# Performance work log

Hardware: AMD Instinct MI355X
Metric: run time of the kernel (lower is better)

Reference implementation:

```python
import jax, jax.numpy as jnp
import numpy as np


def _build_levels():
    # build_power_value(B=4): w_bit=5 -> B=4 additive-powers-of-two codebook
    value_a = [0.0] + [2.0 ** (-2 * i - 1) for i in range(3)]
    value_b = [0.0] + [2.0 ** (-2 * i - 2) for i in range(3)]
    sums = sorted({a + b for a in value_a for b in value_b})
    levels = np.asarray(sums, dtype=np.float32)
    return jnp.asarray(levels / levels.max())  # 16 levels in [0, 1]


def setup_inputs() -> dict:
    key = jax.random.key(0)
    weight = jax.random.normal(key, (4096, 4096), dtype=jnp.float32) * 0.05
    wgt_alpha = jnp.asarray(2.0, dtype=jnp.float32)
    return {"weight": weight, "wgt_alpha": wgt_alpha}


def reference(weight, wgt_alpha):
    levels = _build_levels()
    # stats are computed on weight.data in torch (detached)
    mean = jax.lax.stop_gradient(jnp.mean(weight))
    std = jax.lax.stop_gradient(jnp.std(weight, ddof=1))  # torch .std() is unbiased
    wn = (weight - mean) / std
    x = wn / wgt_alpha
    xc = jnp.clip(x, -1.0, 1.0)
    sign = jnp.sign(xc)
    # nearest-level search over the 16-entry codebook (first-min tie-break like torch)
    idx = jnp.argmin(jnp.abs(jnp.abs(xc)[..., None] - levels), axis=-1)
    q = levels[idx] * sign
    return q * wgt_alpha
```

## Files before the change

### kernel.cpp

```cpp
#include <hip/hip_runtime.h>
#include <math.h>

#define THREADS 256

typedef float f2v __attribute__((ext_vector_type(2)));
typedef float f4v __attribute__((ext_vector_type(4)));

static constexpr float kLvl[16] = {
    0.0f      / 0.75f, 0.015625f / 0.75f, 0.03125f / 0.75f, 0.046875f / 0.75f,
    0.0625f   / 0.75f, 0.09375f  / 0.75f, 0.125f   / 0.75f, 0.140625f / 0.75f,
    0.1875f   / 0.75f, 0.25f     / 0.75f, 0.28125f / 0.75f, 0.375f    / 0.75f,
    0.5f      / 0.75f, 0.515625f / 0.75f, 0.5625f  / 0.75f, 0.75f     / 0.75f,
};
static constexpr double kMid[15] = {
    ((double)kLvl[0]  + (double)kLvl[1])  * 0.5, ((double)kLvl[1]  + (double)kLvl[2])  * 0.5,
    ((double)kLvl[2]  + (double)kLvl[3])  * 0.5, ((double)kLvl[3]  + (double)kLvl[4])  * 0.5,
    ((double)kLvl[4]  + (double)kLvl[5])  * 0.5, ((double)kLvl[5]  + (double)kLvl[6])  * 0.5,
    ((double)kLvl[6]  + (double)kLvl[7])  * 0.5, ((double)kLvl[7]  + (double)kLvl[8])  * 0.5,
    ((double)kLvl[8]  + (double)kLvl[9])  * 0.5, ((double)kLvl[9]  + (double)kLvl[10]) * 0.5,
    ((double)kLvl[10] + (double)kLvl[11]) * 0.5, ((double)kLvl[11] + (double)kLvl[12]) * 0.5,
    ((double)kLvl[12] + (double)kLvl[13]) * 0.5, ((double)kLvl[13] + (double)kLvl[14]) * 0.5,
    ((double)kLvl[14] + (double)kLvl[15]) * 0.5,
};

__device__ __forceinline__ float tree64(float v) {
    #pragma unroll
    for (int m = 1; m <= 32; m <<= 1)
        v += __shfl_xor(v, m, 64);
    return v;
}

__device__ __forceinline__ float sgpr_bcast(float x) {
    return __uint_as_float(__builtin_amdgcn_readfirstlane(__float_as_uint(x)));
}

template<int PASS>
__global__ __launch_bounds__(THREADS) void leaf_pass(const float* __restrict__ w,
                                                     const float* __restrict__ bprev,
                                                     float* __restrict__ bout,
                                                     long long n, int nb) {
    #pragma clang fp contract(off)
    __shared__ float ws4[4];
    __shared__ float smean;
    float mean = 0.0f;
    if (PASS == 1) {
        int i0 = threadIdx.x * 8;
        float v = 0.0f;
        if (i0 + 7 < nb) {
            const float* p = bprev + i0;
            v = ((p[0] + p[1]) + (p[2] + p[3])) + ((p[4] + p[5]) + (p[6] + p[7]));
        }
        v = tree64(v);
        if ((threadIdx.x & 63) == 0) ws4[threadIdx.x >> 6] = v;
        __syncthreads();
        if (threadIdx.x == 0)
            smean = ((ws4[0] + ws4[1]) + (ws4[2] + ws4[3])) / (float)n;
        __syncthreads();
        mean = smean;
    }

    const long long base = (long long)blockIdx.x * 8192
                         + (long long)(threadIdx.x >> 2) * 128
                         + (long long)(threadIdx.x & 3) * 2;
    const f2v* p = (const f2v*)(w + base);
    float s0, s1;
    {
        f2v a = p[0];
        if (PASS == 1) { float x = a.x - mean, y = a.y - mean; s0 = x * x; s1 = y * y; }
        else           { s0 = a.x; s1 = a.y; }
    }
    #pragma unroll
    for (int t = 1; t < 16; ++t) {
        f2v a = p[4 * t];
        if (PASS == 1) { float x = a.x - mean, y = a.y - mean; s0 += x * x; s1 += y * y; }
        else           { s0 += a.x; s1 += a.y; }
    }
    float s = s0 + s1;
    s = tree64(s);
    if ((threadIdx.x & 63) == 0) ws4[threadIdx.x >> 6] = s;
    __syncthreads();
    if (threadIdx.x == 0)
        bout[blockIdx.x] = (ws4[0] + ws4[1]) + (ws4[2] + ws4[3]);
}

#define QSEL(V, RES) do {                                   \
    float _u  = (V) - mean;                                 \
    float _au = fabsf(_u);                                  \
    float _o  = c0;                                         \
    _o = (_au < t0)  ? _o : c1;                             \
    _o = (_au < t1)  ? _o : c2;                             \
    _o = (_au < t2)  ? _o : c3;                             \
    _o = (_au < t3)  ? _o : c4;                             \
    _o = (_au < t4)  ? _o : c5;                             \
    _o = (_au < t5)  ? _o : c6;                             \
    _o = (_au < t6)  ? _o : c7;                             \
    _o = (_au < t7)  ? _o : c8;                             \
    _o = (_au < t8)  ? _o : c9;                             \
    _o = (_au < t9)  ? _o : c10;                            \
    _o = (_au < t10) ? _o : c11;                            \
    _o = (_au < t11) ? _o : c12;                            \
    _o = (_au < t12) ? _o : c13;                            \
    _o = (_au < t13) ? _o : c14;                            \
    _o = (_au < t14) ? _o : c15;                            \
    RES = copysignf(_o, _u);                                \
} while (0)

__global__ __launch_bounds__(THREADS) void quantize_k(const f4v* __restrict__ w4,
                                                      f4v* __restrict__ o4,
                                                      const float* __restrict__ bout0,
                                                      const float* __restrict__ bout1,
                                                      const float* __restrict__ alpha_ptr,
                                                      long long n, int nb) {
    #pragma clang fp contract(off)
    __shared__ float wsA[4], wsB[4];
    __shared__ float sP[2];
    __shared__ float sT[15];
    __shared__ float sC[16];
    {
        int i0 = threadIdx.x * 8;
        float v = 0.0f, u = 0.0f;
        if (i0 + 7 < nb) {
            const float* p0 = bout0 + i0;
            const float* p1 = bout1 + i0;
            v = ((p0[0] + p0[1]) + (p0[2] + p0[3])) + ((p0[4] + p0[5]) + (p0[6] + p0[7]));
            u = ((p1[0] + p1[1]) + (p1[2] + p1[3])) + ((p1[4] + p1[5]) + (p1[6] + p1[7]));
        }
        v = tree64(v);
        u = tree64(u);
        if ((threadIdx.x & 63) == 0) { wsA[threadIdx.x >> 6] = v; wsB[threadIdx.x >> 6] = u; }
        __syncthreads();
        if (threadIdx.x == 0) {
            sP[0] = ((wsA[0] + wsA[1]) + (wsA[2] + wsA[3])) / (float)n;
            sP[1] = sqrtf(((wsB[0] + wsB[1]) + (wsB[2] + wsB[3])) / (float)(n - 1));
        }
        __syncthreads();
    }
    const float sd = sP[1];
    const float al = alpha_ptr[0];
    if (threadIdx.x < 15) {
        const double mid = kMid[threadIdx.x];
        unsigned lo = 0u, hi = 0x7F800000u;
        while (lo < hi) {
            unsigned m = (lo + hi) >> 1;
            float uu = __uint_as_float(m);
            float y  = uu / sd;
            float x  = y / al;
            float xc = fminf(x, 1.0f);
            if ((double)xc > mid) hi = m; else lo = m + 1;
        }
        sT[threadIdx.x] = __uint_as_float(lo);
    } else if (threadIdx.x < 31) {
        int i = threadIdx.x - 15;
        sC[i] = kLvl[i] * al;
    } else if (threadIdx.x == 31) {
        sC[0] = 0.0f;
    }
    __syncthreads();

    const float mean = sgpr_bcast(sP[0]);
    const float t0  = sgpr_bcast(sT[0]),  t1  = sgpr_bcast(sT[1]);
    const float t2  = sgpr_bcast(sT[2]),  t3  = sgpr_bcast(sT[3]);
    const float t4  = sgpr_bcast(sT[4]),  t5  = sgpr_bcast(sT[5]);
    const float t6  = sgpr_bcast(sT[6]),  t7  = sgpr_bcast(sT[7]);
    const float t8  = sgpr_bcast(sT[8]),  t9  = sgpr_bcast(sT[9]);
    const float t10 = sgpr_bcast(sT[10]), t11 = sgpr_bcast(sT[11]);
    const float t12 = sgpr_bcast(sT[12]), t13 = sgpr_bcast(sT[13]);
    const float t14 = sgpr_bcast(sT[14]);
    const float c0  = sgpr_bcast(sC[0]),  c1  = sgpr_bcast(sC[1]);
    const float c2  = sgpr_bcast(sC[2]),  c3  = sgpr_bcast(sC[3]);
    const float c4  = sgpr_bcast(sC[4]),  c5  = sgpr_bcast(sC[5]);
    const float c6  = sgpr_bcast(sC[6]),  c7  = sgpr_bcast(sC[7]);
    const float c8  = sgpr_bcast(sC[8]),  c9  = sgpr_bcast(sC[9]);
    const float c10 = sgpr_bcast(sC[10]), c11 = sgpr_bcast(sC[11]);
    const float c12 = sgpr_bcast(sC[12]), c13 = sgpr_bcast(sC[13]);
    const float c14 = sgpr_bcast(sC[14]), c15 = sgpr_bcast(sC[15]);

    long long n4     = n >> 2;
    long long tid    = (long long)blockIdx.x * THREADS + threadIdx.x;
    long long stride = (long long)gridDim.x * THREADS;

    long long i = tid;
    for (; i + stride < n4; i += 2 * stride) {
        f4v a = w4[i];
        f4v b = w4[i + stride];
        f4v ra, rb;
        QSEL(a.x, ra.x); QSEL(a.y, ra.y); QSEL(a.z, ra.z); QSEL(a.w, ra.w);
        QSEL(b.x, rb.x); QSEL(b.y, rb.y); QSEL(b.z, rb.z); QSEL(b.w, rb.w);
        __builtin_nontemporal_store(ra, &o4[i]);
        __builtin_nontemporal_store(rb, &o4[i + stride]);
    }
    for (; i < n4; i += stride) {
        f4v a = w4[i];
        f4v ra;
        QSEL(a.x, ra.x); QSEL(a.y, ra.y); QSEL(a.z, ra.z); QSEL(a.w, ra.w);
        __builtin_nontemporal_store(ra, &o4[i]);
    }
}

extern "C" void kernel_launch(void* const* d_in, const int* in_sizes, int n_in,
                              void* d_out, int out_size, void* d_ws, size_t ws_size,
                              hipStream_t stream) {
    const float* w     = (const float*)d_in[0];
    const float* alpha = (const float*)d_in[1];
    float* out = (float*)d_out;
    long long n = (long long)in_sizes[0];

    int nblk = (int)(n >> 13);
    float* bout0 = (float*)d_ws;
    float* bout1 = bout0 + nblk;

    leaf_pass<0><<<nblk, THREADS, 0, stream>>>(w, nullptr, bout0, n, nblk);
    leaf_pass<1><<<nblk, THREADS, 0, stream>>>(w, bout0, bout1, n, nblk);
    quantize_k<<<2048, THREADS, 0, stream>>>((const f4v*)w, (f4v*)out,
                                             bout0, bout1, alpha, n, nblk);
}
```

Measured before the change: 54.96 us.

## Fuse mean, std and quantize into one persistent kernel with grid barriers

```diff
diff --git a/kernel.cpp b/kernel.cpp
--- a/kernel.cpp
+++ b/kernel.cpp
@@ -2,6 +2,7 @@
 #include <math.h>
 
 #define THREADS 256
+#define NBLK 512
 
 typedef float f2v __attribute__((ext_vector_type(2)));
 typedef float f4v __attribute__((ext_vector_type(4)));
@@ -34,54 +35,10 @@
     return __uint_as_float(__builtin_amdgcn_readfirstlane(__float_as_uint(x)));
 }
 
-template<int PASS>
-__global__ __launch_bounds__(THREADS) void leaf_pass(const float* __restrict__ w,
-                                                     const float* __restrict__ bprev,
-                                                     float* __restrict__ bout,
-                                                     long long n, int nb) {
-    #pragma clang fp contract(off)
-    __shared__ float ws4[4];
-    __shared__ float smean;
-    float mean = 0.0f;
-    if (PASS == 1) {
-        int i0 = threadIdx.x * 8;
-        float v = 0.0f;
-        if (i0 + 7 < nb) {
-            const float* p = bprev + i0;
-            v = ((p[0] + p[1]) + (p[2] + p[3])) + ((p[4] + p[5]) + (p[6] + p[7]));
-        }
-        v = tree64(v);
-        if ((threadIdx.x & 63) == 0) ws4[threadIdx.x >> 6] = v;
-        __syncthreads();
-        if (threadIdx.x == 0)
-            smean = ((ws4[0] + ws4[1]) + (ws4[2] + ws4[3])) / (float)n;
-        __syncthreads();
-        mean = smean;
-    }
-
-    const long long base = (long long)blockIdx.x * 8192
-                         + (long long)(threadIdx.x >> 2) * 128
-                         + (long long)(threadIdx.x & 3) * 2;
-    const f2v* p = (const f2v*)(w + base);
-    float s0, s1;
-    {
-        f2v a = p[0];
-        if (PASS == 1) { float x = a.x - mean, y = a.y - mean; s0 = x * x; s1 = y * y; }
-        else           { s0 = a.x; s1 = a.y; }
-    }
-    #pragma unroll
-    for (int t = 1; t < 16; ++t) {
-        f2v a = p[4 * t];
-        if (PASS == 1) { float x = a.x - mean, y = a.y - mean; s0 += x * x; s1 += y * y; }
-        else           { s0 += a.x; s1 += a.y; }
-    }
-    float s = s0 + s1;
-    s = tree64(s);
-    if ((threadIdx.x & 63) == 0) ws4[threadIdx.x >> 6] = s;
-    __syncthreads();
-    if (threadIdx.x == 0)
-        bout[blockIdx.x] = (ws4[0] + ws4[1]) + (ws4[2] + ws4[3]);
-}
+#define K15(OP,G) OP(G,1) OP(G,2) OP(G,3) OP(G,4) OP(G,5) OP(G,6) OP(G,7) \
+                  OP(G,8) OP(G,9) OP(G,10) OP(G,11) OP(G,12) OP(G,13) OP(G,14) OP(G,15)
+#define K16(OP,G) OP(G,0) K15(OP,G)
+#define ALLGK(OP) K16(OP,0) K16(OP,1) K16(OP,2) K16(OP,3)
 
 #define QSEL(V, RES) do {                                   \
     float _u  = (V) - mean;                                 \
@@ -105,6 +62,229 @@
     RES = copysignf(_o, _u);                                \
 } while (0)
 
+#define HOIST_TC()                                                        \
+    const float t0  = sgpr_bcast(sT[0]),  t1  = sgpr_bcast(sT[1]);        \
+    const float t2  = sgpr_bcast(sT[2]),  t3  = sgpr_bcast(sT[3]);        \
+    const float t4  = sgpr_bcast(sT[4]),  t5  = sgpr_bcast(sT[5]);        \
+    const float t6  = sgpr_bcast(sT[6]),  t7  = sgpr_bcast(sT[7]);        \
+    const float t8  = sgpr_bcast(sT[8]),  t9  = sgpr_bcast(sT[9]);        \
+    const float t10 = sgpr_bcast(sT[10]), t11 = sgpr_bcast(sT[11]);       \
+    const float t12 = sgpr_bcast(sT[12]), t13 = sgpr_bcast(sT[13]);       \
+    const float t14 = sgpr_bcast(sT[14]);                                 \
+    const float c0  = sgpr_bcast(sC[0]),  c1  = sgpr_bcast(sC[1]);        \
+    const float c2  = sgpr_bcast(sC[2]),  c3  = sgpr_bcast(sC[3]);        \
+    const float c4  = sgpr_bcast(sC[4]),  c5  = sgpr_bcast(sC[5]);        \
+    const float c6  = sgpr_bcast(sC[6]),  c7  = sgpr_bcast(sC[7]);        \
+    const float c8  = sgpr_bcast(sC[8]),  c9  = sgpr_bcast(sC[9]);        \
+    const float c10 = sgpr_bcast(sC[10]), c11 = sgpr_bcast(sC[11]);       \
+    const float c12 = sgpr_bcast(sC[12]), c13 = sgpr_bcast(sC[13]);       \
+    const float c14 = sgpr_bcast(sC[14]), c15 = sgpr_bcast(sC[15]);
+
+#define THRESH_SETUP(TID)                                                 \
+    if ((TID) < 15) {                                                     \
+        const double mid = kMid[(TID)];                                   \
+        unsigned lo = 0u, hi = 0x7F800000u;                               \
+        while (lo < hi) {                                                 \
+            unsigned m = (lo + hi) >> 1;                                  \
+            float uu = __uint_as_float(m);                                \
+            float y  = uu / sd;                                           \
+            float x  = y / al;                                            \
+            float xc = fminf(x, 1.0f);                                    \
+            if ((double)xc > mid) hi = m; else lo = m + 1;                \
+        }                                                                 \
+        sT[(TID)] = __uint_as_float(lo);                                  \
+    } else if ((TID) < 31) {                                              \
+        sC[(TID) - 15] = kLvl[(TID) - 15] * al;                           \
+    } else if ((TID) == 31) {                                             \
+        sC[0] = 0.0f;                                                     \
+    }
+
+__global__ __launch_bounds__(THREADS, 2) void fused_all(const float* __restrict__ w,
+                                                        float* __restrict__ out,
+                                                        const float* __restrict__ alpha_ptr,
+                                                        int* __restrict__ cnt,
+                                                        float* __restrict__ wsum,
+                                                        float* __restrict__ wsq) {
+    #pragma clang fp contract(off)
+    const int t  = threadIdx.x;
+    const int bx = blockIdx.x;
+
+    __shared__ float sh[4];
+    __shared__ float sMean, sSd;
+    __shared__ float sT[15], sC[16];
+
+    const long long base = (long long)bx * 32768
+                         + (long long)(t >> 2) * 512 + (long long)(t & 3) * 2;
+    const f2v* pw = (const f2v*)(w + base);
+
+    #define DECLV(G,K) f2v v##G##_##K = pw[G*64 + K*4];
+    ALLGK(DECLV)
+    #undef DECLV
+
+    {
+        f2v a0 = v0_0, a1 = v1_0, a2 = v2_0, a3 = v3_0;
+        #define ACC1(G,K) a##G += v##G##_##K;
+        K15(ACC1,0) K15(ACC1,1) K15(ACC1,2) K15(ACC1,3)
+        #undef ACC1
+        float s0 = a0.x + a0.y, s1 = a1.x + a1.y;
+        float s2 = a2.x + a2.y, s3 = a3.x + a3.y;
+        float L0 = s0 + __shfl_xor(s0, 1, 64); L0 = L0 + __shfl_xor(L0, 2, 64);
+        float L1 = s1 + __shfl_xor(s1, 1, 64); L1 = L1 + __shfl_xor(L1, 2, 64);
+        float L2 = s2 + __shfl_xor(s2, 1, 64); L2 = L2 + __shfl_xor(L2, 2, 64);
+        float L3 = s3 + __shfl_xor(s3, 1, 64); L3 = L3 + __shfl_xor(L3, 2, 64);
+        float nd = (L0 + L1) + (L2 + L3);
+        nd = nd + __shfl_xor(nd, 4, 64);
+        nd = nd + __shfl_xor(nd, 8, 64);
+        nd = nd + __shfl_xor(nd, 16, 64);
+        nd = nd + __shfl_xor(nd, 32, 64);
+        if ((t & 63) == 0) sh[t >> 6] = nd;
+    }
+    __syncthreads();
+    if (t == 0) {
+        float p = (sh[0] + sh[1]) + (sh[2] + sh[3]);
+        __hip_atomic_store(&wsum[bx], p, __ATOMIC_RELAXED, __HIP_MEMORY_SCOPE_AGENT);
+        __hip_atomic_fetch_add(&cnt[0], 1, __ATOMIC_RELEASE, __HIP_MEMORY_SCOPE_AGENT);
+        while (__hip_atomic_load(&cnt[0], __ATOMIC_ACQUIRE, __HIP_MEMORY_SCOPE_AGENT) < NBLK)
+            __builtin_amdgcn_s_sleep(2);
+    }
+    __syncthreads();
+
+    {
+        float g = 0.0f;
+        if (t < 128) {
+            float p0 = __hip_atomic_load(&wsum[4*t+0], __ATOMIC_RELAXED, __HIP_MEMORY_SCOPE_AGENT);
+            float p1 = __hip_atomic_load(&wsum[4*t+1], __ATOMIC_RELAXED, __HIP_MEMORY_SCOPE_AGENT);
+            float p2 = __hip_atomic_load(&wsum[4*t+2], __ATOMIC_RELAXED, __HIP_MEMORY_SCOPE_AGENT);
+            float p3 = __hip_atomic_load(&wsum[4*t+3], __ATOMIC_RELAXED, __HIP_MEMORY_SCOPE_AGENT);
+            g = (p0 + p1) + (p2 + p3);
+        }
+        g = tree64(g);
+        if ((t & 63) == 0) sh[t >> 6] = g;
+        __syncthreads();
+        if (t == 0) sMean = ((sh[0] + sh[1]) + (sh[2] + sh[3])) / 16777216.0f;
+        __syncthreads();
+    }
+    const float mean = sgpr_bcast(sMean);
+
+    {
+        f2v m2; m2.x = mean; m2.y = mean;
+        f2v d;
+        d = v0_0 - m2; f2v q0 = d * d;
+        d = v1_0 - m2; f2v q1v = d * d;
+        d = v2_0 - m2; f2v q2 = d * d;
+        d = v3_0 - m2; f2v q3 = d * d;
+        #define ACC2_0(G,K) d = v##G##_##K - m2; q0  += d * d;
+        #define ACC2_1(G,K) d = v##G##_##K - m2; q1v += d * d;
+        #define ACC2_2(G,K) d = v##G##_##K - m2; q2  += d * d;
+        #define ACC2_3(G,K) d = v##G##_##K - m2; q3  += d * d;
+        K15(ACC2_0,0) K15(ACC2_1,1) K15(ACC2_2,2) K15(ACC2_3,3)
+        #undef ACC2_0
+        #undef ACC2_1
+        #undef ACC2_2
+        #undef ACC2_3
+        float s0 = q0.x + q0.y, s1 = q1v.x + q1v.y;
+        float s2 = q2.x + q2.y, s3 = q3.x + q3.y;
+        float L0 = s0 + __shfl_xor(s0, 1, 64); L0 = L0 + __shfl_xor(L0, 2, 64);
+        float L1 = s1 + __shfl_xor(s1, 1, 64); L1 = L1 + __shfl_xor(L1, 2, 64);
+        float L2 = s2 + __shfl_xor(s2, 1, 64); L2 = L2 + __shfl_xor(L2, 2, 64);
+        float L3 = s3 + __shfl_xor(s3, 1, 64); L3 = L3 + __shfl_xor(L3, 2, 64);
+        float nd = (L0 + L1) + (L2 + L3);
+        nd = nd + __shfl_xor(nd, 4, 64);
+        nd = nd + __shfl_xor(nd, 8, 64);
+        nd = nd + __shfl_xor(nd, 16, 64);
+        nd = nd + __shfl_xor(nd, 32, 64);
+        if ((t & 63) == 0) sh[t >> 6] = nd;
+    }
+    __syncthreads();
+    if (t == 0) {
+        float p = (sh[0] + sh[1]) + (sh[2] + sh[3]);
+        __hip_atomic_store(&wsq[bx], p, __ATOMIC_RELAXED, __HIP_MEMORY_SCOPE_AGENT);
+        __hip_atomic_fetch_add(&cnt[1], 1, __ATOMIC_RELEASE, __HIP_MEMORY_SCOPE_AGENT);
+        while (__hip_atomic_load(&cnt[1], __ATOMIC_ACQUIRE, __HIP_MEMORY_SCOPE_AGENT) < NBLK)
+            __builtin_amdgcn_s_sleep(2);
+    }
+    __syncthreads();
+
+    {
+        float g = 0.0f;
+        if (t < 128) {
+            float p0 = __hip_atomic_load(&wsq[4*t+0], __ATOMIC_RELAXED, __HIP_MEMORY_SCOPE_AGENT);
+            float p1 = __hip_atomic_load(&wsq[4*t+1], __ATOMIC_RELAXED, __HIP_MEMORY_SCOPE_AGENT);
+            float p2 = __hip_atomic_load(&wsq[4*t+2], __ATOMIC_RELAXED, __HIP_MEMORY_SCOPE_AGENT);
+            float p3 = __hip_atomic_load(&wsq[4*t+3], __ATOMIC_RELAXED, __HIP_MEMORY_SCOPE_AGENT);
+            g = (p0 + p1) + (p2 + p3);
+        }
+        g = tree64(g);
+        if ((t & 63) == 0) sh[t >> 6] = g;
+        __syncthreads();
+        if (t == 0) sSd = sqrtf(((sh[0] + sh[1]) + (sh[2] + sh[3])) / 16777215.0f);
+        __syncthreads();
+    }
+    {
+        const float sd = sSd;
+        const float al = alpha_ptr[0];
+        THRESH_SETUP(t)
+    }
+    __syncthreads();
+
+    HOIST_TC()
+
+    f2v* po = (f2v*)(out + base);
+    #define QST(G,K) { f2v r;                                      \
+        QSEL(v##G##_##K.x, r.x); QSEL(v##G##_##K.y, r.y);          \
+        __builtin_nontemporal_store(r, &po[G*64 + K*4]); }
+    ALLGK(QST)
+    #undef QST
+}
+
+template<int PASS>
+__global__ __launch_bounds__(THREADS) void leaf_pass(const float* __restrict__ w,
+                                                     const float* __restrict__ bprev,
+                                                     float* __restrict__ bout,
+                                                     long long n, int nb) {
+    #pragma clang fp contract(off)
+    __shared__ float ws4[4];
+    __shared__ float smean;
+    float mean = 0.0f;
+    if (PASS == 1) {
+        int i0 = threadIdx.x * 8;
+        float v = 0.0f;
+        if (i0 + 7 < nb) {
+            const float* p = bprev + i0;
+            v = ((p[0] + p[1]) + (p[2] + p[3])) + ((p[4] + p[5]) + (p[6] + p[7]));
+        }
+        v = tree64(v);
+        if ((threadIdx.x & 63) == 0) ws4[threadIdx.x >> 6] = v;
+        __syncthreads();
+        if (threadIdx.x == 0)
+            smean = ((ws4[0] + ws4[1]) + (ws4[2] + ws4[3])) / (float)n;
+        __syncthreads();
+        mean = smean;
+    }
+    const long long base = (long long)blockIdx.x * 8192
+                         + (long long)(threadIdx.x >> 2) * 128
+                         + (long long)(threadIdx.x & 3) * 2;
+    const f2v* p = (const f2v*)(w + base);
+    float s0, s1;
+    {
+        f2v a = p[0];
+        if (PASS == 1) { float x = a.x - mean, y = a.y - mean; s0 = x * x; s1 = y * y; }
+        else           { s0 = a.x; s1 = a.y; }
+    }
+    #pragma unroll
+    for (int t = 1; t < 16; ++t) {
+        f2v a = p[4 * t];
+        if (PASS == 1) { float x = a.x - mean, y = a.y - mean; s0 += x * x; s1 += y * y; }
+        else           { s0 += a.x; s1 += a.y; }
+    }
+    float s = s0 + s1;
+    s = tree64(s);
+    if ((threadIdx.x & 63) == 0) ws4[threadIdx.x >> 6] = s;
+    __syncthreads();
+    if (threadIdx.x == 0)
+        bout[blockIdx.x] = (ws4[0] + ws4[1]) + (ws4[2] + ws4[3]);
+}
+
 __global__ __launch_bounds__(THREADS) void quantize_k(const f4v* __restrict__ w4,
                                                       f4v* __restrict__ o4,
                                                       const float* __restrict__ bout0,
@@ -135,45 +315,15 @@
         }
         __syncthreads();
     }
-    const float sd = sP[1];
-    const float al = alpha_ptr[0];
-    if (threadIdx.x < 15) {
-        const double mid = kMid[threadIdx.x];
-        unsigned lo = 0u, hi = 0x7F800000u;
-        while (lo < hi) {
-            unsigned m = (lo + hi) >> 1;
-            float uu = __uint_as_float(m);
-            float y  = uu / sd;
-            float x  = y / al;
-            float xc = fminf(x, 1.0f);
-            if ((double)xc > mid) hi = m; else lo = m + 1;
-        }
-        sT[threadIdx.x] = __uint_as_float(lo);
-    } else if (threadIdx.x < 31) {
-        int i = threadIdx.x - 15;
-        sC[i] = kLvl[i] * al;
-    } else if (threadIdx.x == 31) {
-        sC[0] = 0.0f;
+    {
+        const float sd = sP[1];
+        const float al = alpha_ptr[0];
+        THRESH_SETUP(threadIdx.x)
     }
     __syncthreads();
 
     const float mean = sgpr_bcast(sP[0]);
-    const float t0  = sgpr_bcast(sT[0]),  t1  = sgpr_bcast(sT[1]);
-    const float t2  = sgpr_bcast(sT[2]),  t3  = sgpr_bcast(sT[3]);
-    const float t4  = sgpr_bcast(sT[4]),  t5  = sgpr_bcast(sT[5]);
-    const float t6  = sgpr_bcast(sT[6]),  t7  = sgpr_bcast(sT[7]);
-    const float t8  = sgpr_bcast(sT[8]),  t9  = sgpr_bcast(sT[9]);
-    const float t10 = sgpr_bcast(sT[10]), t11 = sgpr_bcast(sT[11]);
-    const float t12 = sgpr_bcast(sT[12]), t13 = sgpr_bcast(sT[13]);
-    const float t14 = sgpr_bcast(sT[14]);
-    const float c0  = sgpr_bcast(sC[0]),  c1  = sgpr_bcast(sC[1]);
-    const float c2  = sgpr_bcast(sC[2]),  c3  = sgpr_bcast(sC[3]);
-    const float c4  = sgpr_bcast(sC[4]),  c5  = sgpr_bcast(sC[5]);
-    const float c6  = sgpr_bcast(sC[6]),  c7  = sgpr_bcast(sC[7]);
-    const float c8  = sgpr_bcast(sC[8]),  c9  = sgpr_bcast(sC[9]);
-    const float c10 = sgpr_bcast(sC[10]), c11 = sgpr_bcast(sC[11]);
-    const float c12 = sgpr_bcast(sC[12]), c13 = sgpr_bcast(sC[13]);
-    const float c14 = sgpr_bcast(sC[14]), c15 = sgpr_bcast(sC[15]);
+    HOIST_TC()
 
     long long n4     = n >> 2;
     long long tid    = (long long)blockIdx.x * THREADS + threadIdx.x;
@@ -205,12 +355,20 @@
     float* out = (float*)d_out;
     long long n = (long long)in_sizes[0];
 
-    int nblk = (int)(n >> 13);
-    float* bout0 = (float*)d_ws;
-    float* bout1 = bout0 + nblk;
-
-    leaf_pass<0><<<nblk, THREADS, 0, stream>>>(w, nullptr, bout0, n, nblk);
-    leaf_pass<1><<<nblk, THREADS, 0, stream>>>(w, bout0, bout1, n, nblk);
-    quantize_k<<<2048, THREADS, 0, stream>>>((const f4v*)w, (f4v*)out,
-                                             bout0, bout1, alpha, n, nblk);
-}
+    size_t need = 2 * sizeof(int) + (size_t)(2 * NBLK) * sizeof(float);
+    if (n == (1LL << 24) && ws_size >= need) {
+        int*   cnt  = (int*)d_ws;
+        float* wsum = (float*)d_ws + 2;
+        float* wsq  = wsum + NBLK;
+        hipMemsetAsync(cnt, 0, 2 * sizeof(int), stream);
+        fused_all<<<NBLK, THREADS, 0, stream>>>(w, out, alpha, cnt, wsum, wsq);
+    } else {
+        int nblk = (int)(n >> 13);
+        float* bout0 = (float*)d_ws;
+        float* bout1 = bout0 + nblk;
+        leaf_pass<0><<<nblk, THREADS, 0, stream>>>(w, nullptr, bout0, n, nblk);
+        leaf_pass<1><<<nblk, THREADS, 0, stream>>>(w, bout0, bout1, n, nblk);
+        quantize_k<<<2048, THREADS, 0, stream>>>((const f4v*)w, (f4v*)out,
+                                                 bout0, bout1, alpha, n, nblk);
+    }
+}
```

New measurement: 170.3 us. +209.8%, slower.

## Split threshold computation into single-block kernel and unroll quantize loop by four

Applied to the files above, without the earlier changes.

```diff
diff --git a/kernel.cpp b/kernel.cpp
--- a/kernel.cpp
+++ b/kernel.cpp
@@ -32,55 +32,6 @@
 
 __device__ __forceinline__ float sgpr_bcast(float x) {
     return __uint_as_float(__builtin_amdgcn_readfirstlane(__float_as_uint(x)));
-}
-
-template<int PASS>
-__global__ __launch_bounds__(THREADS) void leaf_pass(const float* __restrict__ w,
-                                                     const float* __restrict__ bprev,
-                                                     float* __restrict__ bout,
-                                                     long long n, int nb) {
-    #pragma clang fp contract(off)
-    __shared__ float ws4[4];
-    __shared__ float smean;
-    float mean = 0.0f;
-    if (PASS == 1) {
-        int i0 = threadIdx.x * 8;
-        float v = 0.0f;
-        if (i0 + 7 < nb) {
-            const float* p = bprev + i0;
-            v = ((p[0] + p[1]) + (p[2] + p[3])) + ((p[4] + p[5]) + (p[6] + p[7]));
-        }
-        v = tree64(v);
-        if ((threadIdx.x & 63) == 0) ws4[threadIdx.x >> 6] = v;
-        __syncthreads();
-        if (threadIdx.x == 0)
-            smean = ((ws4[0] + ws4[1]) + (ws4[2] + ws4[3])) / (float)n;
-        __syncthreads();
-        mean = smean;
-    }
-
-    const long long base = (long long)blockIdx.x * 8192
-                         + (long long)(threadIdx.x >> 2) * 128
-                         + (long long)(threadIdx.x & 3) * 2;
-    const f2v* p = (const f2v*)(w + base);
-    float s0, s1;
-    {
-        f2v a = p[0];
-        if (PASS == 1) { float x = a.x - mean, y = a.y - mean; s0 = x * x; s1 = y * y; }
-        else           { s0 = a.x; s1 = a.y; }
-    }
-    #pragma unroll
-    for (int t = 1; t < 16; ++t) {
-        f2v a = p[4 * t];
-        if (PASS == 1) { float x = a.x - mean, y = a.y - mean; s0 += x * x; s1 += y * y; }
-        else           { s0 += a.x; s1 += a.y; }
-    }
-    float s = s0 + s1;
-    s = tree64(s);
-    if ((threadIdx.x & 63) == 0) ws4[threadIdx.x >> 6] = s;
-    __syncthreads();
-    if (threadIdx.x == 0)
-        bout[blockIdx.x] = (ws4[0] + ws4[1]) + (ws4[2] + ws4[3]);
 }
 
 #define QSEL(V, RES) do {                                   \
@@ -105,17 +56,80 @@
     RES = copysignf(_o, _u);                                \
 } while (0)
 
-__global__ __launch_bounds__(THREADS) void quantize_k(const f4v* __restrict__ w4,
-                                                      f4v* __restrict__ o4,
-                                                      const float* __restrict__ bout0,
-                                                      const float* __restrict__ bout1,
-                                                      const float* __restrict__ alpha_ptr,
-                                                      long long n, int nb) {
+#define HOIST_TC(SRC)                                                     \
+    const float t0  = sgpr_bcast(SRC[1]),  t1  = sgpr_bcast(SRC[2]);      \
+    const float t2  = sgpr_bcast(SRC[3]),  t3  = sgpr_bcast(SRC[4]);      \
+    const float t4  = sgpr_bcast(SRC[5]),  t5  = sgpr_bcast(SRC[6]);      \
+    const float t6  = sgpr_bcast(SRC[7]),  t7  = sgpr_bcast(SRC[8]);      \
+    const float t8  = sgpr_bcast(SRC[9]),  t9  = sgpr_bcast(SRC[10]);     \
+    const float t10 = sgpr_bcast(SRC[11]), t11 = sgpr_bcast(SRC[12]);     \
+    const float t12 = sgpr_bcast(SRC[13]), t13 = sgpr_bcast(SRC[14]);     \
+    const float t14 = sgpr_bcast(SRC[15]);                                \
+    const float c0  = sgpr_bcast(SRC[16]), c1  = sgpr_bcast(SRC[17]);     \
+    const float c2  = sgpr_bcast(SRC[18]), c3  = sgpr_bcast(SRC[19]);     \
+    const float c4  = sgpr_bcast(SRC[20]), c5  = sgpr_bcast(SRC[21]);     \
+    const float c6  = sgpr_bcast(SRC[22]), c7  = sgpr_bcast(SRC[23]);     \
+    const float c8  = sgpr_bcast(SRC[24]), c9  = sgpr_bcast(SRC[25]);     \
+    const float c10 = sgpr_bcast(SRC[26]), c11 = sgpr_bcast(SRC[27]);     \
+    const float c12 = sgpr_bcast(SRC[28]), c13 = sgpr_bcast(SRC[29]);     \
+    const float c14 = sgpr_bcast(SRC[30]), c15 = sgpr_bcast(SRC[31]);
+
+template<int PASS>
+__global__ __launch_bounds__(THREADS) void leaf_pass(const float* __restrict__ w,
+                                                     const float* __restrict__ bprev,
+                                                     float* __restrict__ bout,
+                                                     long long n, int nb) {
+    #pragma clang fp contract(off)
+    __shared__ float ws4[4];
+    __shared__ float smean;
+    float mean = 0.0f;
+    if (PASS == 1) {
+        int i0 = threadIdx.x * 8;
+        float v = 0.0f;
+        if (i0 + 7 < nb) {
+            const float* p = bprev + i0;
+            v = ((p[0] + p[1]) + (p[2] + p[3])) + ((p[4] + p[5]) + (p[6] + p[7]));
+        }
+        v = tree64(v);
+        if ((threadIdx.x & 63) == 0) ws4[threadIdx.x >> 6] = v;
+        __syncthreads();
+        if (threadIdx.x == 0)
+            smean = ((ws4[0] + ws4[1]) + (ws4[2] + ws4[3])) / (float)n;
+        __syncthreads();
+        mean = smean;
+    }
+    const long long base = (long long)blockIdx.x * 8192
+                         + (long long)(threadIdx.x >> 2) * 128
+                         + (long long)(threadIdx.x & 3) * 2;
+    const f2v* p = (const f2v*)(w + base);
+    float s0, s1;
+    {
+        f2v a = p[0];
+        if (PASS == 1) { float x = a.x - mean, y = a.y - mean; s0 = x * x; s1 = y * y; }
+        else           { s0 = a.x; s1 = a.y; }
+    }
+    #pragma unroll
+    for (int t = 1; t < 16; ++t) {
+        f2v a = p[4 * t];
+        if (PASS == 1) { float x = a.x - mean, y = a.y - mean; s0 += x * x; s1 += y * y; }
+        else           { s0 += a.x; s1 += a.y; }
+    }
+    float s = s0 + s1;
+    s = tree64(s);
+    if ((threadIdx.x & 63) == 0) ws4[threadIdx.x >> 6] = s;
+    __syncthreads();
+    if (threadIdx.x == 0)
+        bout[blockIdx.x] = (ws4[0] + ws4[1]) + (ws4[2] + ws4[3]);
+}
+
+__global__ __launch_bounds__(THREADS) void finz(const float* __restrict__ bout0,
+                                                const float* __restrict__ bout1,
+                                                const float* __restrict__ alpha_ptr,
+                                                long long n, int nb,
+                                                float* __restrict__ params) {
     #pragma clang fp contract(off)
     __shared__ float wsA[4], wsB[4];
-    __shared__ float sP[2];
-    __shared__ float sT[15];
-    __shared__ float sC[16];
+    __shared__ float sMean, sSd;
     {
         int i0 = threadIdx.x * 8;
         float v = 0.0f, u = 0.0f;
@@ -130,15 +144,17 @@
         if ((threadIdx.x & 63) == 0) { wsA[threadIdx.x >> 6] = v; wsB[threadIdx.x >> 6] = u; }
         __syncthreads();
         if (threadIdx.x == 0) {
-            sP[0] = ((wsA[0] + wsA[1]) + (wsA[2] + wsA[3])) / (float)n;
-            sP[1] = sqrtf(((wsB[0] + wsB[1]) + (wsB[2] + wsB[3])) / (float)(n - 1));
-        }
-        __syncthreads();
-    }
-    const float sd = sP[1];
+            sMean = ((wsA[0] + wsA[1]) + (wsA[2] + wsA[3])) / (float)n;
+            sSd   = sqrtf(((wsB[0] + wsB[1]) + (wsB[2] + wsB[3])) / (float)(n - 1));
+        }
+        __syncthreads();
+    }
+    const float sd = sSd;
     const float al = alpha_ptr[0];
-    if (threadIdx.x < 15) {
-        const double mid = kMid[threadIdx.x];
+    const int t = threadIdx.x;
+    if (t == 32) params[0] = sMean;
+    if (t < 15) {
+        const double mid = kMid[t];
         unsigned lo = 0u, hi = 0x7F800000u;
         while (lo < hi) {
             unsigned m = (lo + hi) >> 1;
@@ -148,52 +164,48 @@
             float xc = fminf(x, 1.0f);
             if ((double)xc > mid) hi = m; else lo = m + 1;
         }
-        sT[threadIdx.x] = __uint_as_float(lo);
-    } else if (threadIdx.x < 31) {
-        int i = threadIdx.x - 15;
-        sC[i] = kLvl[i] * al;
-    } else if (threadIdx.x == 31) {
-        sC[0] = 0.0f;
-    }
+        params[1 + t] = __uint_as_float(lo);
+    } else if (t >= 16 && t < 32) {
+        int i = t - 16;
+        params[16 + i] = (i == 0) ? 0.0f : kLvl[i] * al;
+    }
+}
+
+__global__ __launch_bounds__(THREADS) void quantize_s(const f4v* __restrict__ w4,
+                                                      f4v* __restrict__ o4,
+                                                      const float* __restrict__ params,
+                                                      long long n4) {
+    #pragma clang fp contract(off)
+    __shared__ float sp[32];
+    if (threadIdx.x < 32) sp[threadIdx.x] = params[threadIdx.x];
     __syncthreads();
-
-    const float mean = sgpr_bcast(sP[0]);
-    const float t0  = sgpr_bcast(sT[0]),  t1  = sgpr_bcast(sT[1]);
-    const float t2  = sgpr_bcast(sT[2]),  t3  = sgpr_bcast(sT[3]);
-    const float t4  = sgpr_bcast(sT[4]),  t5  = sgpr_bcast(sT[5]);
-    const float t6  = sgpr_bcast(sT[6]),  t7  = sgpr_bcast(sT[7]);
-    const float t8  = sgpr_bcast(sT[8]),  t9  = sgpr_bcast(sT[9]);
-    const float t10 = sgpr_bcast(sT[10]), t11 = sgpr_bcast(sT[11]);
-    const float t12 = sgpr_bcast(sT[12]), t13 = sgpr_bcast(sT[13]);
-    const float t14 = sgpr_bcast(sT[14]);
-    const float c0  = sgpr_bcast(sC[0]),  c1  = sgpr_bcast(sC[1]);
-    const float c2  = sgpr_bcast(sC[2]),  c3  = sgpr_bcast(sC[3]);
-    const float c4  = sgpr_bcast(sC[4]),  c5  = sgpr_bcast(sC[5]);
-    const float c6  = sgpr_bcast(sC[6]),  c7  = sgpr_bcast(sC[7]);
-    const float c8  = sgpr_bcast(sC[8]),  c9  = sgpr_bcast(sC[9]);
-    const float c10 = sgpr_bcast(sC[10]), c11 = sgpr_bcast(sC[11]);
-    const float c12 = sgpr_bcast(sC[12]), c13 = sgpr_bcast(sC[13]);
-    const float c14 = sgpr_bcast(sC[14]), c15 = sgpr_bcast(sC[15]);
-
-    long long n4     = n >> 2;
+    const float mean = sgpr_bcast(sp[0]);
+    HOIST_TC(sp)
+
     long long tid    = (long long)blockIdx.x * THREADS + threadIdx.x;
     long long stride = (long long)gridDim.x * THREADS;
 
     long long i = tid;
-    for (; i + stride < n4; i += 2 * stride) {
+    for (; i + 3 * stride < n4; i += 4 * stride) {
         f4v a = w4[i];
         f4v b = w4[i + stride];
-        f4v ra, rb;
+        f4v c = w4[i + 2 * stride];
+        f4v d = w4[i + 3 * stride];
+        f4v ra, rb, rc, rd;
         QSEL(a.x, ra.x); QSEL(a.y, ra.y); QSEL(a.z, ra.z); QSEL(a.w, ra.w);
         QSEL(b.x, rb.x); QSEL(b.y, rb.y); QSEL(b.z, rb.z); QSEL(b.w, rb.w);
-        __builtin_nontemporal_store(ra, &o4[i]);
-        __builtin_nontemporal_store(rb, &o4[i + stride]);
+        QSEL(c.x, rc.x); QSEL(c.y, rc.y); QSEL(c.z, rc.z); QSEL(c.w, rc.w);
+        QSEL(d.x, rd.x); QSEL(d.y, rd.y); QSEL(d.z, rd.z); QSEL(d.w, rd.w);
+        o4[i]              = ra;
+        o4[i + stride]     = rb;
+        o4[i + 2 * stride] = rc;
+        o4[i + 3 * stride] = rd;
     }
     for (; i < n4; i += stride) {
         f4v a = w4[i];
         f4v ra;
         QSEL(a.x, ra.x); QSEL(a.y, ra.y); QSEL(a.z, ra.z); QSEL(a.w, ra.w);
-        __builtin_nontemporal_store(ra, &o4[i]);
+        o4[i] = ra;
     }
 }
 
@@ -206,11 +218,12 @@
     long long n = (long long)in_sizes[0];
 
     int nblk = (int)(n >> 13);
-    float* bout0 = (float*)d_ws;
-    float* bout1 = bout0 + nblk;
+    float* bout0  = (float*)d_ws;
+    float* bout1  = bout0 + nblk;
+    float* params = bout1 + nblk;
 
     leaf_pass<0><<<nblk, THREADS, 0, stream>>>(w, nullptr, bout0, n, nblk);
     leaf_pass<1><<<nblk, THREADS, 0, stream>>>(w, bout0, bout1, n, nblk);
-    quantize_k<<<2048, THREADS, 0, stream>>>((const f4v*)w, (f4v*)out,
-                                             bout0, bout1, alpha, n, nblk);
-}
+    finz<<<1, THREADS, 0, stream>>>(bout0, bout1, alpha, n, nblk, params);
+    quantize_s<<<2048, THREADS, 0, stream>>>((const f4v*)w, (f4v*)out, params, n >> 2);
+}
```

Result: slower. 57.64 us (+4.9%).

## Reverse second stats pass order and use one-shot block quantize kernel

Applied to the files above, without the earlier changes.

```diff
diff --git a/kernel.cpp b/kernel.cpp
--- a/kernel.cpp
+++ b/kernel.cpp
@@ -32,55 +32,6 @@
 
 __device__ __forceinline__ float sgpr_bcast(float x) {
     return __uint_as_float(__builtin_amdgcn_readfirstlane(__float_as_uint(x)));
-}
-
-template<int PASS>
-__global__ __launch_bounds__(THREADS) void leaf_pass(const float* __restrict__ w,
-                                                     const float* __restrict__ bprev,
-                                                     float* __restrict__ bout,
-                                                     long long n, int nb) {
-    #pragma clang fp contract(off)
-    __shared__ float ws4[4];
-    __shared__ float smean;
-    float mean = 0.0f;
-    if (PASS == 1) {
-        int i0 = threadIdx.x * 8;
-        float v = 0.0f;
-        if (i0 + 7 < nb) {
-            const float* p = bprev + i0;
-            v = ((p[0] + p[1]) + (p[2] + p[3])) + ((p[4] + p[5]) + (p[6] + p[7]));
-        }
-        v = tree64(v);
-        if ((threadIdx.x & 63) == 0) ws4[threadIdx.x >> 6] = v;
-        __syncthreads();
-        if (threadIdx.x == 0)
-            smean = ((ws4[0] + ws4[1]) + (ws4[2] + ws4[3])) / (float)n;
-        __syncthreads();
-        mean = smean;
-    }
-
-    const long long base = (long long)blockIdx.x * 8192
-                         + (long long)(threadIdx.x >> 2) * 128
-                         + (long long)(threadIdx.x & 3) * 2;
-    const f2v* p = (const f2v*)(w + base);
-    float s0, s1;
-    {
-        f2v a = p[0];
-        if (PASS == 1) { float x = a.x - mean, y = a.y - mean; s0 = x * x; s1 = y * y; }
-        else           { s0 = a.x; s1 = a.y; }
-    }
-    #pragma unroll
-    for (int t = 1; t < 16; ++t) {
-        f2v a = p[4 * t];
-        if (PASS == 1) { float x = a.x - mean, y = a.y - mean; s0 += x * x; s1 += y * y; }
-        else           { s0 += a.x; s1 += a.y; }
-    }
-    float s = s0 + s1;
-    s = tree64(s);
-    if ((threadIdx.x & 63) == 0) ws4[threadIdx.x >> 6] = s;
-    __syncthreads();
-    if (threadIdx.x == 0)
-        bout[blockIdx.x] = (ws4[0] + ws4[1]) + (ws4[2] + ws4[3]);
 }
 
 #define QSEL(V, RES) do {                                   \
@@ -105,7 +56,97 @@
     RES = copysignf(_o, _u);                                \
 } while (0)
 
-__global__ __launch_bounds__(THREADS) void quantize_k(const f4v* __restrict__ w4,
+#define HOIST_TC()                                                        \
+    const float t0  = sgpr_bcast(sT[0]),  t1  = sgpr_bcast(sT[1]);        \
+    const float t2  = sgpr_bcast(sT[2]),  t3  = sgpr_bcast(sT[3]);        \
+    const float t4  = sgpr_bcast(sT[4]),  t5  = sgpr_bcast(sT[5]);        \
+    const float t6  = sgpr_bcast(sT[6]),  t7  = sgpr_bcast(sT[7]);        \
+    const float t8  = sgpr_bcast(sT[8]),  t9  = sgpr_bcast(sT[9]);        \
+    const float t10 = sgpr_bcast(sT[10]), t11 = sgpr_bcast(sT[11]);       \
+    const float t12 = sgpr_bcast(sT[12]), t13 = sgpr_bcast(sT[13]);       \
+    const float t14 = sgpr_bcast(sT[14]);                                 \
+    const float c0  = sgpr_bcast(sC[0]),  c1  = sgpr_bcast(sC[1]);        \
+    const float c2  = sgpr_bcast(sC[2]),  c3  = sgpr_bcast(sC[3]);        \
+    const float c4  = sgpr_bcast(sC[4]),  c5  = sgpr_bcast(sC[5]);        \
+    const float c6  = sgpr_bcast(sC[6]),  c7  = sgpr_bcast(sC[7]);        \
+    const float c8  = sgpr_bcast(sC[8]),  c9  = sgpr_bcast(sC[9]);        \
+    const float c10 = sgpr_bcast(sC[10]), c11 = sgpr_bcast(sC[11]);       \
+    const float c12 = sgpr_bcast(sC[12]), c13 = sgpr_bcast(sC[13]);       \
+    const float c14 = sgpr_bcast(sC[14]), c15 = sgpr_bcast(sC[15]);
+
+#define THRESH_SETUP(TID)                                                 \
+    if ((TID) < 15) {                                                     \
+        const double mid = kMid[(TID)];                                   \
+        unsigned lo = 0u, hi = 0x7F800000u;                               \
+        while (lo < hi) {                                                 \
+            unsigned m = (lo + hi) >> 1;                                  \
+            float uu = __uint_as_float(m);                                \
+            float y  = uu / sd;                                           \
+            float x  = y / al;                                            \
+            float xc = fminf(x, 1.0f);                                    \
+            if ((double)xc > mid) hi = m; else lo = m + 1;                \
+        }                                                                 \
+        sT[(TID)] = __uint_as_float(lo);                                  \
+    } else if ((TID) < 31) {                                              \
+        sC[(TID) - 15] = kLvl[(TID) - 15] * al;                           \
+    } else if ((TID) == 31) {                                             \
+        sC[0] = 0.0f;                                                     \
+    }
+
+template<int PASS, int REV>
+__global__ __launch_bounds__(THREADS) void leaf_pass(const float* __restrict__ w,
+                                                     const float* __restrict__ bprev,
+                                                     float* __restrict__ bout,
+                                                     long long n, int nb) {
+    #pragma clang fp contract(off)
+    __shared__ float ws4[4];
+    __shared__ float smean;
+    float mean = 0.0f;
+    if (PASS == 1) {
+        int i0 = threadIdx.x * 8;
+        float v = 0.0f;
+        if (i0 + 7 < nb) {
+            const float* p = bprev + i0;
+            v = ((p[0] + p[1]) + (p[2] + p[3])) + ((p[4] + p[5]) + (p[6] + p[7]));
+        }
+        v = tree64(v);
+        if ((threadIdx.x & 63) == 0) ws4[threadIdx.x >> 6] = v;
+        __syncthreads();
+        if (threadIdx.x == 0)
+            smean = ((ws4[0] + ws4[1]) + (ws4[2] + ws4[3])) / (float)n;
+        __syncthreads();
+        mean = smean;
+    }
+    int region = blockIdx.x;
+    if (REV && (nb & 7) == 0) {
+        int j = blockIdx.x >> 3;
+        region = (blockIdx.x & 7) + 8 * ((nb >> 3) - 1 - j);
+    }
+    const long long base = (long long)region * 8192
+                         + (long long)(threadIdx.x >> 2) * 128
+                         + (long long)(threadIdx.x & 3) * 2;
+    const f2v* p = (const f2v*)(w + base);
+    float s0, s1;
+    {
+        f2v a = p[0];
+        if (PASS == 1) { float x = a.x - mean, y = a.y - mean; s0 = x * x; s1 = y * y; }
+        else           { s0 = a.x; s1 = a.y; }
+    }
+    #pragma unroll
+    for (int t = 1; t < 16; ++t) {
+        f2v a = p[4 * t];
+        if (PASS == 1) { float x = a.x - mean, y = a.y - mean; s0 += x * x; s1 += y * y; }
+        else           { s0 += a.x; s1 += a.y; }
+    }
+    float s = s0 + s1;
+    s = tree64(s);
+    if ((threadIdx.x & 63) == 0) ws4[threadIdx.x >> 6] = s;
+    __syncthreads();
+    if (threadIdx.x == 0)
+        bout[region] = (ws4[0] + ws4[1]) + (ws4[2] + ws4[3]);
+}
+
+__global__ __launch_bounds__(THREADS) void quantize_b(const f4v* __restrict__ w4,
                                                       f4v* __restrict__ o4,
                                                       const float* __restrict__ bout0,
                                                       const float* __restrict__ bout1,
@@ -135,50 +176,87 @@
         }
         __syncthreads();
     }
-    const float sd = sP[1];
-    const float al = alpha_ptr[0];
-    if (threadIdx.x < 15) {
-        const double mid = kMid[threadIdx.x];
-        unsigned lo = 0u, hi = 0x7F800000u;
-        while (lo < hi) {
-            unsigned m = (lo + hi) >> 1;
-            float uu = __uint_as_float(m);
-            float y  = uu / sd;
-            float x  = y / al;
-            float xc = fminf(x, 1.0f);
-            if ((double)xc > mid) hi = m; else lo = m + 1;
-        }
-        sT[threadIdx.x] = __uint_as_float(lo);
-    } else if (threadIdx.x < 31) {
-        int i = threadIdx.x - 15;
-        sC[i] = kLvl[i] * al;
-    } else if (threadIdx.x == 31) {
-        sC[0] = 0.0f;
+    {
+        const float sd = sP[1];
+        const float al = alpha_ptr[0];
+        THRESH_SETUP(threadIdx.x)
     }
     __syncthreads();
 
     const float mean = sgpr_bcast(sP[0]);
-    const float t0  = sgpr_bcast(sT[0]),  t1  = sgpr_bcast(sT[1]);
-    const float t2  = sgpr_bcast(sT[2]),  t3  = sgpr_bcast(sT[3]);
-    const float t4  = sgpr_bcast(sT[4]),  t5  = sgpr_bcast(sT[5]);
-    const float t6  = sgpr_bcast(sT[6]),  t7  = sgpr_bcast(sT[7]);
-    const float t8  = sgpr_bcast(sT[8]),  t9  = sgpr_bcast(sT[9]);
-    const float t10 = sgpr_bcast(sT[10]), t11 = sgpr_bcast(sT[11]);
-    const float t12 = sgpr_bcast(sT[12]), t13 = sgpr_bcast(sT[13]);
-    const float t14 = sgpr_bcast(sT[14]);
-    const float c0  = sgpr_bcast(sC[0]),  c1  = sgpr_bcast(sC[1]);
-    const float c2  = sgpr_bcast(sC[2]),  c3  = sgpr_bcast(sC[3]);
-    const float c4  = sgpr_bcast(sC[4]),  c5  = sgpr_bcast(sC[5]);
-    const float c6  = sgpr_bcast(sC[6]),  c7  = sgpr_bcast(sC[7]);
-    const float c8  = sgpr_bcast(sC[8]),  c9  = sgpr_bcast(sC[9]);
-    const float c10 = sgpr_bcast(sC[10]), c11 = sgpr_bcast(sC[11]);
-    const float c12 = sgpr_bcast(sC[12]), c13 = sgpr_bcast(sC[13]);
-    const float c14 = sgpr_bcast(sC[14]), c15 = sgpr_bcast(sC[15]);
+    HOIST_TC()
+
+    const long long base = (long long)blockIdx.x * 2048 + threadIdx.x;
+    f4v a0 = w4[base];
+    f4v a1 = w4[base + 256];
+    f4v a2 = w4[base + 512];
+    f4v a3 = w4[base + 768];
+    f4v a4 = w4[base + 1024];
+    f4v a5 = w4[base + 1280];
+    f4v a6 = w4[base + 1536];
+    f4v a7 = w4[base + 1792];
+    f4v r;
+    QSEL(a0.x, r.x); QSEL(a0.y, r.y); QSEL(a0.z, r.z); QSEL(a0.w, r.w);
+    __builtin_nontemporal_store(r, &o4[base]);
+    QSEL(a1.x, r.x); QSEL(a1.y, r.y); QSEL(a1.z, r.z); QSEL(a1.w, r.w);
+    __builtin_nontemporal_store(r, &o4[base + 256]);
+    QSEL(a2.x, r.x); QSEL(a2.y, r.y); QSEL(a2.z, r.z); QSEL(a2.w, r.w);
+    __builtin_nontemporal_store(r, &o4[base + 512]);
+    QSEL(a3.x, r.x); QSEL(a3.y, r.y); QSEL(a3.z, r.z); QSEL(a3.w, r.w);
+    __builtin_nontemporal_store(r, &o4[base + 768]);
+    QSEL(a4.x, r.x); QSEL(a4.y, r.y); QSEL(a4.z, r.z); QSEL(a4.w, r.w);
+    __builtin_nontemporal_store(r, &o4[base + 1024]);
+    QSEL(a5.x, r.x); QSEL(a5.y, r.y); QSEL(a5.z, r.z); QSEL(a5.w, r.w);
+    __builtin_nontemporal_store(r, &o4[base + 1280]);
+    QSEL(a6.x, r.x); QSEL(a6.y, r.y); QSEL(a6.z, r.z); QSEL(a6.w, r.w);
+    __builtin_nontemporal_store(r, &o4[base + 1536]);
+    QSEL(a7.x, r.x); QSEL(a7.y, r.y); QSEL(a7.z, r.z); QSEL(a7.w, r.w);
+    __builtin_nontemporal_store(r, &o4[base + 1792]);
+}
+
+__global__ __launch_bounds__(THREADS) void quantize_g(const f4v* __restrict__ w4,
+                                                      f4v* __restrict__ o4,
+                                                      const float* __restrict__ bout0,
+                                                      const float* __restrict__ bout1,
+                                                      const float* __restrict__ alpha_ptr,
+                                                      long long n, int nb) {
+    #pragma clang fp contract(off)
+    __shared__ float wsA[4], wsB[4];
+    __shared__ float sP[2];
+    __shared__ float sT[15];
+    __shared__ float sC[16];
+    {
+        int i0 = threadIdx.x * 8;
+        float v = 0.0f, u = 0.0f;
+        if (i0 + 7 < nb) {
+            const float* p0 = bout0 + i0;
+            const float* p1 = bout1 + i0;
+            v = ((p0[0] + p0[1]) + (p0[2] + p0[3])) + ((p0[4] + p0[5]) + (p0[6] + p0[7]));
+            u = ((p1[0] + p1[1]) + (p1[2] + p1[3])) + ((p1[4] + p1[5]) + (p1[6] + p1[7]));
+        }
+        v = tree64(v);
+        u = tree64(u);
+        if ((threadIdx.x & 63) == 0) { wsA[threadIdx.x >> 6] = v; wsB[threadIdx.x >> 6] = u; }
+        __syncthreads();
+        if (threadIdx.x == 0) {
+            sP[0] = ((wsA[0] + wsA[1]) + (wsA[2] + wsA[3])) / (float)n;
+            sP[1] = sqrtf(((wsB[0] + wsB[1]) + (wsB[2] + wsB[3])) / (float)(n - 1));
+        }
+        __syncthreads();
+    }
+    {
+        const float sd = sP[1];
+        const float al = alpha_ptr[0];
+        THRESH_SETUP(threadIdx.x)
+    }
+    __syncthreads();
+
+    const float mean = sgpr_bcast(sP[0]);
+    HOIST_TC()
 
     long long n4     = n >> 2;
     long long tid    = (long long)blockIdx.x * THREADS + threadIdx.x;
     long long stride = (long long)gridDim.x * THREADS;
-
     long long i = tid;
     for (; i + stride < n4; i += 2 * stride) {
         f4v a = w4[i];
@@ -209,8 +287,13 @@
     float* bout0 = (float*)d_ws;
     float* bout1 = bout0 + nblk;
 
-    leaf_pass<0><<<nblk, THREADS, 0, stream>>>(w, nullptr, bout0, n, nblk);
-    leaf_pass<1><<<nblk, THREADS, 0, stream>>>(w, bout0, bout1, n, nblk);
-    quantize_k<<<2048, THREADS, 0, stream>>>((const f4v*)w, (f4v*)out,
-                                             bout0, bout1, alpha, n, nblk);
-}
+    leaf_pass<0, 0><<<nblk, THREADS, 0, stream>>>(w, nullptr, bout0, n, nblk);
+    leaf_pass<1, 1><<<nblk, THREADS, 0, stream>>>(w, bout0, bout1, n, nblk);
+    if (n == (1LL << 24)) {
+        quantize_b<<<nblk, THREADS, 0, stream>>>((const f4v*)w, (f4v*)out,
+                                                 bout0, bout1, alpha, n, nblk);
+    } else {
+        quantize_g<<<2048, THREADS, 0, stream>>>((const f4v*)w, (f4v*)out,
+                                                 bout0, bout1, alpha, n, nblk);
+    }
+}
```

New measurement: 52.70 us. 1.04x faster.
